# Optimization experiments

Hardware: AMD Instinct MI355X
Metric: run time of the kernel (lower is better)

Reference implementation:

```python
import jax, jax.numpy as jnp
import numpy as np
from functools import reduce

N_QUBITS = 12          # input_shape[-2] = 2**12 = 4096; must be multiple of 4
DIM = 2 ** N_QUBITS
N_GATES = N_QUBITS // 4  # one diamond U-gate (4 qubits, 16x16) per group
BATCH = 128
TWO_PI = 6.283185307179586


def setup_inputs() -> dict:
    key = jax.random.key(0)
    k1, k2, k3, k4 = jax.random.split(key, 4)
    thetas = jax.random.uniform(k1, (N_GATES,), jnp.float32, 0.0, TWO_PI)
    # Fixed Hermitian generator for the 16x16 gate, pre-diagonalized:
    # U(theta) = V @ diag(exp(-i*theta*evals)) @ V^T
    rng = np.random.RandomState(42)
    H = rng.randn(16, 16).astype(np.float32)
    H = (H + H.T) * 0.5
    evals_np, evecs_np = np.linalg.eigh(H)
    evecs = jnp.asarray(evecs_np, jnp.float32)
    evals = jnp.asarray(evals_np, jnp.float32)
    state_real = jax.random.normal(k3, (BATCH, DIM, 1), jnp.float32)
    state_imag = jax.random.normal(k4, (BATCH, DIM, 1), jnp.float32)
    return {"thetas": thetas, "evecs": evecs, "evals": evals,
            "state_real": state_real, "state_imag": state_imag}


def _gate(theta, evecs, evals):
    # 16x16 unitary: V diag(exp(-i theta lambda)) V^T  (V real orthogonal)
    phase = jnp.exp(-1j * (theta * evals).astype(jnp.complex64))  # [16]
    V = evecs.astype(jnp.complex64)
    return (V * phase[None, :]) @ V.T  # [16,16] complex64


def reference(thetas, evecs, evals, state_real, state_imag):
    # Build each 4-qubit gate, then the full unitary via Kronecker product
    Us = [_gate(thetas[i], evecs, evals) for i in range(N_GATES)]
    U_full = reduce(jnp.kron, Us)  # [DIM, DIM] complex64 (the anti-pattern)
    psi = state_real.astype(jnp.complex64) + 1j * state_imag.astype(jnp.complex64)
    out = jnp.einsum('ij,bjk->bik', U_full, psi)  # U @ inputs
    # stack real/imag so output is a single real array: [2, BATCH, DIM, 1]
    return jnp.stack([jnp.real(out), jnp.imag(out)])
```

## Files before the change

### kernel.cpp

```cpp
#include <hip/hip_runtime.h>

#define DIM 4096
#define NB 128
#define NT 512
#define S1 17
#define S0 274

__global__ __launch_bounds__(NT)
void ulayer_kernel(const float* __restrict__ thetas,
                   const float* __restrict__ evecs,
                   const float* __restrict__ evals,
                   const float* __restrict__ sre,
                   const float* __restrict__ sim,
                   float* __restrict__ out)
{
    __shared__ float  sV[256];
    __shared__ float  sC[48];
    __shared__ float  sS[48];
    __shared__ float2 sG[3][16][16];
    __shared__ float2 st[16 * S0];

    const int t = threadIdx.x;
    const int b = blockIdx.x;

    if (t < 256) sV[t] = evecs[t];
    else if (t < 304) {
        const int e = t - 256;
        const int g = e >> 4, k = e & 15;
        float sn, cs;
        sincosf(thetas[g] * evals[k], &sn, &cs);
        sC[e] = cs;
        sS[e] = sn;
    }

    const float4* __restrict__ vre = (const float4*)(sre + (size_t)b * DIM);
    const float4* __restrict__ vim = (const float4*)(sim + (size_t)b * DIM);
    float4 lre[2], lim[2];
#pragma unroll
    for (int it = 0; it < 2; ++it) {
        lre[it] = vre[t + NT * it];
        lim[it] = vim[t + NT * it];
    }

    __syncthreads();

#pragma unroll
    for (int rep = 0; rep < 2; ++rep) {
        const int e = t + (rep << 9);
        if (e < 768) {
            const int g = e >> 8;
            const int i = (e >> 4) & 15;
            const int j = e & 15;
            float gr = 0.f, gi = 0.f;
#pragma unroll
            for (int k = 0; k < 16; ++k) {
                const float vv = sV[i * 16 + k] * sV[j * 16 + k];
                gr = fmaf(vv,  sC[(g << 4) + k], gr);
                gi = fmaf(vv, -sS[(g << 4) + k], gi);
            }
            sG[g][i][j] = make_float2(gr, gi);
        }
    }

#pragma unroll
    for (int it = 0; it < 2; ++it) {
        const int e0 = (t + NT * it) << 2;
        const int i0 = e0 >> 8;
        const int r  = e0 & 255;
        const int base = i0 * S0 + (r >> 4) * S1 + (r & 15);
        const float* pr = (const float*)&lre[it];
        const float* pi = (const float*)&lim[it];
#pragma unroll
        for (int q = 0; q < 4; ++q)
            st[base + q] = make_float2(pr[q], pi[q]);
    }
    __syncthreads();

    const int fg = t & 63;
    const int ih = t >> 6;
    const int r0 = ih * 2;

    auto pass = [&](const int gidx, const int BH, const int BK, const int STRIDE) {
        float2 g0[16], g1[16];
#pragma unroll
        for (int j = 0; j < 16; ++j) {
            g0[j] = sG[gidx][r0][j];
            g1[j] = sG[gidx][r0 + 1][j];
        }
        float2 y0[4], y1[4];
#pragma unroll
        for (int fl = 0; fl < 4; ++fl) {
            const int f = fg + 64 * fl;
            const int h = f >> 4;
            const int k = f & 15;
            const int base = h * BH + k * BK;
            float2 x[16];
#pragma unroll
            for (int j = 0; j < 16; ++j) x[j] = st[base + j * STRIDE];
            float ar0 = 0.f, ai0 = 0.f, ar1 = 0.f, ai1 = 0.f;
#pragma unroll
            for (int j = 0; j < 16; ++j) {
                ar0 = fmaf(g0[j].x,  x[j].x, ar0);
                ar0 = fmaf(-g0[j].y, x[j].y, ar0);
                ai0 = fmaf(g0[j].x,  x[j].y, ai0);
                ai0 = fmaf(g0[j].y,  x[j].x, ai0);
                ar1 = fmaf(g1[j].x,  x[j].x, ar1);
                ar1 = fmaf(-g1[j].y, x[j].y, ar1);
                ai1 = fmaf(g1[j].x,  x[j].y, ai1);
                ai1 = fmaf(g1[j].y,  x[j].x, ai1);
            }
            y0[fl] = make_float2(ar0, ai0);
            y1[fl] = make_float2(ar1, ai1);
        }
        __syncthreads();
#pragma unroll
        for (int fl = 0; fl < 4; ++fl) {
            const int f = fg + 64 * fl;
            const int h = f >> 4;
            const int k = f & 15;
            const int base = h * BH + k * BK;
            st[base + r0 * STRIDE]       = y0[fl];
            st[base + (r0 + 1) * STRIDE] = y1[fl];
        }
        __syncthreads();
    };

    pass(2, S0, S1, 1);
    pass(1, S0, 1, S1);
    pass(0, S1, 1, S0);

    float* __restrict__ ore = out + (size_t)b * DIM;
    float* __restrict__ oim = out + (size_t)NB * DIM + (size_t)b * DIM;
#pragma unroll
    for (int it = 0; it < 2; ++it) {
        const int e0 = (t + NT * it) << 2;
        const int i0 = e0 >> 8;
        const int r  = e0 & 255;
        const int base = i0 * S0 + (r >> 4) * S1 + (r & 15);
        float4 xr, xi;
        float* qr = (float*)&xr;
        float* qi = (float*)&xi;
#pragma unroll
        for (int q = 0; q < 4; ++q) {
            const float2 v = st[base + q];
            qr[q] = v.x;
            qi[q] = v.y;
        }
        *(float4*)(ore + e0) = xr;
        *(float4*)(oim + e0) = xi;
    }
}

extern "C" void kernel_launch(void* const* d_in, const int* in_sizes, int n_in,
                              void* d_out, int out_size, void* d_ws, size_t ws_size,
                              hipStream_t stream) {
    const float* thetas = (const float*)d_in[0];
    const float* evecs  = (const float*)d_in[1];
    const float* evals  = (const float*)d_in[2];
    const float* sre    = (const float*)d_in[3];
    const float* sim    = (const float*)d_in[4];
    float* out = (float*)d_out;
    ulayer_kernel<<<NB, NT, 0, stream>>>(thetas, evecs, evals, sre, sim, out);
}
```

Before: 71.31 us.

## Split gate application into two kernels for more blocks across batch

Replaces the single kernel that ran one block per batch element with two kernels. The first applies gates 2 and 1 on 256-element chunks, using 2048 blocks. The second applies gate 0 across the strided dimension, using 512 blocks and reading the intermediate from a workspace buffer. The aim is to fill more compute units than 128 blocks can, since the old kernel left most CUs idle. The cost is a second launch, a global round trip of the intermediate state, and recomputing the gate matrices in every block.

```diff
diff --git a/kernel.cpp b/kernel.cpp
--- a/kernel.cpp
+++ b/kernel.cpp
@@ -2,152 +2,156 @@
 
 #define DIM 4096
 #define NB 128
-#define NT 512
-#define S1 17
-#define S0 274
 
-__global__ __launch_bounds__(NT)
-void ulayer_kernel(const float* __restrict__ thetas,
-                   const float* __restrict__ evecs,
-                   const float* __restrict__ evals,
-                   const float* __restrict__ sre,
-                   const float* __restrict__ sim,
-                   float* __restrict__ out)
+__global__ __launch_bounds__(256)
+void ulayer_a(const float* __restrict__ thetas,
+              const float* __restrict__ evecs,
+              const float* __restrict__ evals,
+              const float* __restrict__ sre,
+              const float* __restrict__ sim,
+              float2* __restrict__ ws)
 {
     __shared__ float  sV[256];
-    __shared__ float  sC[48];
-    __shared__ float  sS[48];
-    __shared__ float2 sG[3][16][16];
-    __shared__ float2 st[16 * S0];
+    __shared__ float  sC[32], sS[32];
+    __shared__ float2 sG1[16][17];
+    __shared__ float2 sG2[16][17];
+    __shared__ float2 x0[16][17];
+    __shared__ float2 x1[16][17];
 
-    const int t = threadIdx.x;
-    const int b = blockIdx.x;
+    const int t  = threadIdx.x;
+    const int b  = blockIdx.x >> 4;
+    const int c  = blockIdx.x & 15;
+    const int i1 = t >> 4;
+    const int i2 = t & 15;
 
-    if (t < 256) sV[t] = evecs[t];
-    else if (t < 304) {
-        const int e = t - 256;
-        const int g = e >> 4, k = e & 15;
+    sV[t] = evecs[t];
+    if (t < 32) {
+        const int g = (t >> 4) + 1;
+        const int k = t & 15;
         float sn, cs;
         sincosf(thetas[g] * evals[k], &sn, &cs);
-        sC[e] = cs;
-        sS[e] = sn;
+        sC[t] = cs;
+        sS[t] = sn;
     }
 
-    const float4* __restrict__ vre = (const float4*)(sre + (size_t)b * DIM);
-    const float4* __restrict__ vim = (const float4*)(sim + (size_t)b * DIM);
-    float4 lre[2], lim[2];
-#pragma unroll
-    for (int it = 0; it < 2; ++it) {
-        lre[it] = vre[t + NT * it];
-        lim[it] = vim[t + NT * it];
-    }
+    const int d = b * DIM + c * 256 + t;
+    const float xr = sre[d];
+    const float xi = sim[d];
+    x0[i1][i2] = make_float2(xr, xi);
 
     __syncthreads();
 
 #pragma unroll
     for (int rep = 0; rep < 2; ++rep) {
-        const int e = t + (rep << 9);
-        if (e < 768) {
-            const int g = e >> 8;
-            const int i = (e >> 4) & 15;
-            const int j = e & 15;
-            float gr = 0.f, gi = 0.f;
+        const int e  = t + (rep << 8);
+        const int gg = e >> 8;
+        const int i  = (e >> 4) & 15;
+        const int j  = e & 15;
+        float gr = 0.f, gi = 0.f;
 #pragma unroll
-            for (int k = 0; k < 16; ++k) {
-                const float vv = sV[i * 16 + k] * sV[j * 16 + k];
-                gr = fmaf(vv,  sC[(g << 4) + k], gr);
-                gi = fmaf(vv, -sS[(g << 4) + k], gi);
-            }
-            sG[g][i][j] = make_float2(gr, gi);
+        for (int k = 0; k < 16; ++k) {
+            const float vv = sV[i * 16 + k] * sV[j * 16 + k];
+            gr = fmaf(vv,  sC[(gg << 4) + k], gr);
+            gi = fmaf(vv, -sS[(gg << 4) + k], gi);
         }
-    }
-
-#pragma unroll
-    for (int it = 0; it < 2; ++it) {
-        const int e0 = (t + NT * it) << 2;
-        const int i0 = e0 >> 8;
-        const int r  = e0 & 255;
-        const int base = i0 * S0 + (r >> 4) * S1 + (r & 15);
-        const float* pr = (const float*)&lre[it];
-        const float* pi = (const float*)&lim[it];
-#pragma unroll
-        for (int q = 0; q < 4; ++q)
-            st[base + q] = make_float2(pr[q], pi[q]);
+        if (gg == 0) sG1[i][j] = make_float2(gr, gi);
+        else         sG2[j][i] = make_float2(gr, gi);
     }
     __syncthreads();
 
-    const int fg = t & 63;
-    const int ih = t >> 6;
-    const int r0 = ih * 2;
-
-    auto pass = [&](const int gidx, const int BH, const int BK, const int STRIDE) {
-        float2 g0[16], g1[16];
+    {
+        float ar = 0.f, ai = 0.f;
 #pragma unroll
         for (int j = 0; j < 16; ++j) {
-            g0[j] = sG[gidx][r0][j];
-            g1[j] = sG[gidx][r0 + 1][j];
+            const float2 g = sG2[j][i2];
+            const float2 x = x0[i1][j];
+            ar = fmaf(g.x,  x.x, ar);
+            ar = fmaf(-g.y, x.y, ar);
+            ai = fmaf(g.x,  x.y, ai);
+            ai = fmaf(g.y,  x.x, ai);
         }
-        float2 y0[4], y1[4];
+        x1[i1][i2] = make_float2(ar, ai);
+    }
+    __syncthreads();
+
+    {
+        float ar = 0.f, ai = 0.f;
 #pragma unroll
-        for (int fl = 0; fl < 4; ++fl) {
-            const int f = fg + 64 * fl;
-            const int h = f >> 4;
-            const int k = f & 15;
-            const int base = h * BH + k * BK;
-            float2 x[16];
+        for (int j = 0; j < 16; ++j) {
+            const float2 g = sG1[i1][j];
+            const float2 x = x1[j][i2];
+            ar = fmaf(g.x,  x.x, ar);
+            ar = fmaf(-g.y, x.y, ar);
+            ai = fmaf(g.x,  x.y, ai);
+            ai = fmaf(g.y,  x.x, ai);
+        }
+        ws[d] = make_float2(ar, ai);
+    }
+}
+
+__global__ __launch_bounds__(256)
+void ulayer_b(const float* __restrict__ thetas,
+              const float* __restrict__ evecs,
+              const float* __restrict__ evals,
+              const float2* __restrict__ ws,
+              float* __restrict__ out)
+{
+    __shared__ float  sV[256];
+    __shared__ float  sC[16], sS[16];
+    __shared__ float2 sG0[16][16];
+
+    const int t  = threadIdx.x;
+    const int b  = blockIdx.x >> 2;
+    const int fp = blockIdx.x & 3;
+    const int q  = t >> 6;
+    const int fl = t & 63;
+    const int f  = fp * 64 + fl;
+
+    float2 x[16];
+    const float2* __restrict__ wsb = ws + (size_t)b * DIM;
 #pragma unroll
-            for (int j = 0; j < 16; ++j) x[j] = st[base + j * STRIDE];
-            float ar0 = 0.f, ai0 = 0.f, ar1 = 0.f, ai1 = 0.f;
+    for (int j = 0; j < 16; ++j) x[j] = wsb[j * 256 + f];
+
+    sV[t] = evecs[t];
+    if (t < 16) {
+        float sn, cs;
+        sincosf(thetas[0] * evals[t], &sn, &cs);
+        sC[t] = cs;
+        sS[t] = sn;
+    }
+    __syncthreads();
+
+    {
+        const int i = t >> 4, j = t & 15;
+        float gr = 0.f, gi = 0.f;
 #pragma unroll
-            for (int j = 0; j < 16; ++j) {
-                ar0 = fmaf(g0[j].x,  x[j].x, ar0);
-                ar0 = fmaf(-g0[j].y, x[j].y, ar0);
-                ai0 = fmaf(g0[j].x,  x[j].y, ai0);
-                ai0 = fmaf(g0[j].y,  x[j].x, ai0);
-                ar1 = fmaf(g1[j].x,  x[j].x, ar1);
-                ar1 = fmaf(-g1[j].y, x[j].y, ar1);
-                ai1 = fmaf(g1[j].x,  x[j].y, ai1);
-                ai1 = fmaf(g1[j].y,  x[j].x, ai1);
-            }
-            y0[fl] = make_float2(ar0, ai0);
-            y1[fl] = make_float2(ar1, ai1);
+        for (int k = 0; k < 16; ++k) {
+            const float vv = sV[i * 16 + k] * sV[j * 16 + k];
+            gr = fmaf(vv,  sC[k], gr);
+            gi = fmaf(vv, -sS[k], gi);
         }
-        __syncthreads();
-#pragma unroll
-        for (int fl = 0; fl < 4; ++fl) {
-            const int f = fg + 64 * fl;
-            const int h = f >> 4;
-            const int k = f & 15;
-            const int base = h * BH + k * BK;
-            st[base + r0 * STRIDE]       = y0[fl];
-            st[base + (r0 + 1) * STRIDE] = y1[fl];
-        }
-        __syncthreads();
-    };
-
-    pass(2, S0, S1, 1);
-    pass(1, S0, 1, S1);
-    pass(0, S1, 1, S0);
+        sG0[i][j] = make_float2(gr, gi);
+    }
+    __syncthreads();
 
     float* __restrict__ ore = out + (size_t)b * DIM;
     float* __restrict__ oim = out + (size_t)NB * DIM + (size_t)b * DIM;
+
 #pragma unroll
-    for (int it = 0; it < 2; ++it) {
-        const int e0 = (t + NT * it) << 2;
-        const int i0 = e0 >> 8;
-        const int r  = e0 & 255;
-        const int base = i0 * S0 + (r >> 4) * S1 + (r & 15);
-        float4 xr, xi;
-        float* qr = (float*)&xr;
-        float* qi = (float*)&xi;
+    for (int r = 0; r < 4; ++r) {
+        const int i0 = q * 4 + r;
+        float ar = 0.f, ai = 0.f;
 #pragma unroll
-        for (int q = 0; q < 4; ++q) {
-            const float2 v = st[base + q];
-            qr[q] = v.x;
-            qi[q] = v.y;
+        for (int j = 0; j < 16; ++j) {
+            const float2 g = sG0[i0][j];
+            ar = fmaf(g.x,  x[j].x, ar);
+            ar = fmaf(-g.y, x[j].y, ar);
+            ai = fmaf(g.x,  x[j].y, ai);
+            ai = fmaf(g.y,  x[j].x, ai);
         }
-        *(float4*)(ore + e0) = xr;
-        *(float4*)(oim + e0) = xi;
+        const int od = i0 * 256 + f;
+        ore[od] = ar;
+        oim[od] = ai;
     }
 }
 
@@ -159,6 +163,9 @@
     const float* evals  = (const float*)d_in[2];
     const float* sre    = (const float*)d_in[3];
     const float* sim    = (const float*)d_in[4];
-    float* out = (float*)d_out;
-    ulayer_kernel<<<NB, NT, 0, stream>>>(thetas, evecs, evals, sre, sim, out);
+    float* outp = (float*)d_out;
+    float2* ws  = (float2*)d_ws;
+
+    ulayer_a<<<NB * 16, 256, 0, stream>>>(thetas, evecs, evals, sre, sim, ws);
+    ulayer_b<<<NB * 4,  256, 0, stream>>>(thetas, evecs, evals, ws, outp);
 }
```

Result: slower. 79.57 us (+11.6%).
